# Kernel tuning notes

Measured on AMD Instinct MI355X. Metric: run time of the kernel, lower is better.

Reference implementation:

```python
import jax, jax.numpy as jnp
import numpy as np


def setup_inputs() -> dict:
    key = jax.random.key(0)
    ks = jax.random.split(key, 6)
    B, T, U = 4, 160, 80
    De, Dd = 640, 640
    inner, vocab = 640, 1024
    return {
        "enc_state": jax.random.normal(ks[0], (B, T, De), jnp.float32),
        "dec_state": jax.random.normal(ks[1], (B, U, Dd), jnp.float32),
        "W1": jax.random.normal(ks[2], (De + Dd, inner), jnp.float32) * (1.0 / np.sqrt(De + Dd)),
        "b1": jax.random.normal(ks[3], (inner,), jnp.float32) * 0.02,
        "W2": jax.random.normal(ks[4], (inner, vocab), jnp.float32) * (1.0 / np.sqrt(inner)),
        "b2": jax.random.normal(ks[5], (vocab,), jnp.float32) * 0.02,
    }


def reference(enc_state, dec_state, W1, b1, W2, b2):
    # Faithful to: cat([enc tiled over U, dec tiled over T], -1) @ W1 + b1,
    # algebraically split so the [B,T,U,2D] concat is never materialized:
    # cat(e, d) @ W1 == e @ W1[:De] + d @ W1[De:]
    De = enc_state.shape[-1]
    W1_enc, W1_dec = W1[:De], W1[De:]
    enc_proj = jnp.einsum("btd,dh->bth", enc_state, W1_enc)   # [B,T,H]
    dec_proj = jnp.einsum("bud,dh->buh", dec_state, W1_dec)   # [B,U,H]
    # broadcast add over the (T,U) lattice -> [B,T,U,H]
    hidden = jnp.tanh(enc_proj[:, :, None, :] + dec_proj[:, None, :, :] + b1)
    logits = jnp.einsum("btuh,hv->btuv", hidden, W2) + b2     # [B,T,U,V]
    return logits
```

## Files before the change

kernel.cpp:

```cpp
#include <hip/hip_runtime.h>
#include <hip/hip_bf16.h>
#include <cstdint>

#define B_    4
#define T_    160
#define U_    80
#define D_    640
#define V_    1024
#define BT_   640
#define BU_   320
#define M_    51200

typedef __bf16 bf16x8 __attribute__((ext_vector_type(8)));
typedef float floatx4 __attribute__((ext_vector_type(4)));

__device__ __forceinline__ void g2l16(const void* g, void* l) {
    __builtin_amdgcn_global_load_lds((const __attribute__((address_space(1))) void*)g,
                                     (__attribute__((address_space(3))) void*)l,
                                     16, 0, 0);
}

__device__ __forceinline__ float fast_tanh(float x) {
    float e = __builtin_amdgcn_exp2f(x * 2.8853900817779268f);
    return 1.0f - 2.0f * __builtin_amdgcn_rcpf(e + 1.0f);
}

__global__ __launch_bounds__(256) void proj_kernel(
    const float* __restrict__ enc, const float* __restrict__ dec,
    const float* __restrict__ W1,
    float* __restrict__ encp, float* __restrict__ decp) {
    __shared__ float As[64][36];
    __shared__ float Ws[32][68];

    const int rt = blockIdx.y;
    const int ct = blockIdx.x;
    const float* Asrc; const float* Wsrc; float* Cdst;
    if (rt < 10) { Asrc = enc + (size_t)rt * 64 * D_;        Wsrc = W1;           Cdst = encp + (size_t)rt * 64 * D_; }
    else         { Asrc = dec + (size_t)(rt - 10) * 64 * D_; Wsrc = W1 + D_ * D_; Cdst = decp + (size_t)(rt - 10) * 64 * D_; }

    const int tid = threadIdx.x;
    const int ar = tid >> 2,  ac = (tid & 3) * 8;
    const int wr2 = tid >> 3, wc2 = (tid & 7) * 8;
    const int tr = tid >> 4,  tc = tid & 15;

    float acc[4][4] = {};
    for (int k0 = 0; k0 < D_; k0 += 32) {
        __syncthreads();
        *(floatx4*)&As[ar][ac]       = *(const floatx4*)&Asrc[(size_t)ar * D_ + k0 + ac];
        *(floatx4*)&As[ar][ac + 4]   = *(const floatx4*)&Asrc[(size_t)ar * D_ + k0 + ac + 4];
        *(floatx4*)&Ws[wr2][wc2]     = *(const floatx4*)&Wsrc[(size_t)(k0 + wr2) * D_ + ct * 64 + wc2];
        *(floatx4*)&Ws[wr2][wc2 + 4] = *(const floatx4*)&Wsrc[(size_t)(k0 + wr2) * D_ + ct * 64 + wc2 + 4];
        __syncthreads();
#pragma unroll
        for (int kk = 0; kk < 32; kk++) {
            floatx4 w = *(const floatx4*)&Ws[kk][tc * 4];
            float a0 = As[tr * 4 + 0][kk], a1 = As[tr * 4 + 1][kk];
            float a2 = As[tr * 4 + 2][kk], a3 = As[tr * 4 + 3][kk];
#pragma unroll
            for (int j = 0; j < 4; j++) {
                acc[0][j] += a0 * w[j]; acc[1][j] += a1 * w[j];
                acc[2][j] += a2 * w[j]; acc[3][j] += a3 * w[j];
            }
        }
    }
#pragma unroll
    for (int i = 0; i < 4; i++) {
        floatx4 v = { acc[i][0], acc[i][1], acc[i][2], acc[i][3] };
        *(floatx4*)&Cdst[(size_t)(tr * 4 + i) * D_ + ct * 64 + tc * 4] = v;
    }
}

__global__ __launch_bounds__(256) void w2t_kernel(
    const float* __restrict__ W2, __bf16* __restrict__ W2t) {
    __shared__ __bf16 tile[32][33];
    const int vt = blockIdx.x;
    const int kt = blockIdx.y;
    const int tx = threadIdx.x & 31, ty = threadIdx.x >> 5;
#pragma unroll
    for (int i = 0; i < 4; i++)
        tile[ty + i * 8][tx] = (__bf16)W2[(size_t)(kt * 32 + ty + i * 8) * V_ + vt * 32 + tx];
    __syncthreads();
#pragma unroll
    for (int i = 0; i < 4; i++)
        W2t[(size_t)(vt * 32 + ty + i * 8) * D_ + kt * 32 + tx] = tile[tx][ty + i * 8];
}

__global__ __launch_bounds__(256) void hidden_kernel(
    const float* __restrict__ encp, const float* __restrict__ decp,
    const float* __restrict__ b1, __bf16* __restrict__ H) {
    const unsigned g = blockIdx.x * 256u + threadIdx.x;
    const unsigned row = g / 80u;
    const unsigned hg  = g % 80u;
    const unsigned u   = row % 80u;
    const unsigned bt  = row / 80u;
    const unsigned b   = bt / 160u;

    const float* ep = encp + (size_t)bt * D_ + hg * 8;
    const float* dp = decp + (size_t)(b * 80u + u) * D_ + hg * 8;
    const float* bp = b1 + hg * 8;

    floatx4 e0 = *(const floatx4*)ep,       e1 = *(const floatx4*)(ep + 4);
    floatx4 d0 = *(const floatx4*)dp,       d1 = *(const floatx4*)(dp + 4);
    floatx4 c0 = *(const floatx4*)bp,       c1 = *(const floatx4*)(bp + 4);

    bf16x8 hv;
#pragma unroll
    for (int i = 0; i < 4; i++) hv[i]     = (__bf16)fast_tanh(e0[i] + d0[i] + c0[i]);
#pragma unroll
    for (int i = 0; i < 4; i++) hv[i + 4] = (__bf16)fast_tanh(e1[i] + d1[i] + c1[i]);

    *(bf16x8*)(H + (size_t)g * 8) = hv;
}

#define VM4  asm volatile("s_waitcnt vmcnt(4)" ::: "memory")
#define VM0  asm volatile("s_waitcnt vmcnt(0)" ::: "memory")
#define BAR  __builtin_amdgcn_s_barrier()
#define SCB  __builtin_amdgcn_sched_barrier(0)

#define STG_A(BUF, S, TL) do { \
    g2l16(Hb + (unsigned)((S)*163840 + (TL)*128) + agl,         ldsp + (BUF)*32768 + (S)*16384 + stl); \
    g2l16(Hb + (unsigned)((S)*163840 + (TL)*128 + 10240) + agl, ldsp + (BUF)*32768 + (S)*16384 + stl + 1024); \
  } while (0)
#define STG_B(BUF, S, TL) do { \
    g2l16(Wb + (unsigned)((S)*163840 + (TL)*128) + agl,         ldsp + 65536 + (BUF)*32768 + (S)*16384 + stl); \
    g2l16(Wb + (unsigned)((S)*163840 + (TL)*128 + 10240) + agl, ldsp + 65536 + (BUF)*32768 + (S)*16384 + stl + 1024); \
  } while (0)

#define RD_A(ABUF, QM) do { \
    _Pragma("unroll") for (int ii = 0; ii < 4; ++ii) { \
      af0[ii] = *(const bf16x8*)(ldsp + (ABUF)*32768 + (QM)*16384 + ii*2048 + aRowB + sx0); \
      af1[ii] = *(const bf16x8*)(ldsp + (ABUF)*32768 + (QM)*16384 + ii*2048 + aRowB + sx1); \
    } } while (0)
#define RD_B(BG0, BG1, BBUF, QN) do { \
    _Pragma("unroll") for (int jj = 0; jj < 2; ++jj) { \
      BG0[jj] = *(const bf16x8*)(ldsp + 65536 + (BBUF)*32768 + (QN)*16384 + jj*2048 + bRowB + sx0); \
      BG1[jj] = *(const bf16x8*)(ldsp + 65536 + (BBUF)*32768 + (QN)*16384 + jj*2048 + bRowB + sx1); \
    } } while (0)
#define MM(QM, QN, BG0, BG1) do { \
    __builtin_amdgcn_s_setprio(1); \
    _Pragma("unroll") for (int ii = 0; ii < 4; ++ii) \
      _Pragma("unroll") for (int jj = 0; jj < 2; ++jj) { \
        acc[(QM)*4+ii][(QN)*2+jj] = __builtin_amdgcn_mfma_f32_16x16x32_bf16(af0[ii], BG0[jj], acc[(QM)*4+ii][(QN)*2+jj], 0, 0, 0); \
        acc[(QM)*4+ii][(QN)*2+jj] = __builtin_amdgcn_mfma_f32_16x16x32_bf16(af1[ii], BG1[jj], acc[(QM)*4+ii][(QN)*2+jj], 0, 0, 0); \
      } \
    __builtin_amdgcn_s_setprio(0); \
  } while (0)

__global__ __launch_bounds__(512, 2) void gemm_kernel(
    const __bf16* __restrict__ H, const __bf16* __restrict__ W2t,
    const float* __restrict__ b2, float* __restrict__ C) {
    __shared__ __align__(128) char lds[131072];

    const int bid = blockIdx.x;
    const int swz = (bid & 7) * 100 + (bid >> 3);
    const int mt = swz >> 2, nt = swz & 3;
    const int m0 = mt * 256, n0 = nt * 256;

    const int tid = threadIdx.x;
    const int w = tid >> 6, l = tid & 63;
    const int wr = w >> 2, wc = w & 3;
    const int lrow = l & 15, lk = l >> 4, l7 = l & 7, lhi = l >> 3;

    const unsigned swzb = (unsigned)(((l & 7) ^ lhi) * 16);
    const unsigned agl  = (unsigned)((w * 16 + lhi) * 1280) + swzb;
    const unsigned stl  = (unsigned)(w * 2048 + l * 16);

    const char* Hb = (const char*)H   + (size_t)m0 * 1280;
    const char* Wb = (const char*)W2t + (size_t)n0 * 1280;
    char* ldsp = (char*)lds;

    const unsigned aRowB = (unsigned)((wr * 64 + lrow) * 128);
    const unsigned bRowB = (unsigned)(wc * 4096 + lrow * 128);
    const unsigned sx0 = (unsigned)(((0 + lk) ^ l7) * 16);
    const unsigned sx1 = (unsigned)(((4 + lk) ^ l7) * 16);

    floatx4 acc[8][4] = {};

    STG_A(0, 0, 0); STG_A(0, 1, 0); STG_B(0, 0, 0); STG_B(0, 1, 0);
    STG_A(1, 0, 1); STG_B(1, 0, 1);
    VM4; BAR; SCB;

#pragma unroll 1
    for (int it = 0; it < 5; ++it) {
        const int t1 = 2 * it + 1, t2 = 2 * it + 2, t3 = 2 * it + 3;
        const bool pf = (it < 4);
        bf16x8 af0[4], af1[4], bgA0[2], bgA1[2], bgB0[2], bgB1[2];

        RD_A(0, 0); RD_B(bgA0, bgA1, 0, 0);
        STG_A(1, 1, t1); STG_B(1, 1, t1);
        BAR; SCB; MM(0, 0, bgA0, bgA1); BAR; SCB;
        RD_B(bgB0, bgB1, 0, 1);
        BAR; SCB; MM(0, 1, bgB0, bgB1); BAR; SCB;
        RD_A(0, 1);
        if (pf) STG_A(0, 0, t2);
        BAR; SCB; MM(1, 0, bgA0, bgA1); BAR; SCB;
        if (pf) STG_B(0, 0, t2);
        if (it == 4) { VM0; } else { VM4; }
        BAR; SCB; MM(1, 1, bgB0, bgB1); BAR; SCB;

        RD_A(1, 0); RD_B(bgA0, bgA1, 1, 0);
        if (pf) { STG_A(0, 1, t2); STG_B(0, 1, t2); }
        BAR; SCB; MM(0, 0, bgA0, bgA1); BAR; SCB;
        RD_B(bgB0, bgB1, 1, 1);
        BAR; SCB; MM(0, 1, bgB0, bgB1); BAR; SCB;
        RD_A(1, 1);
        if (pf) STG_A(1, 0, t3);
        BAR; SCB; MM(1, 0, bgA0, bgA1); BAR; SCB;
        if (pf) STG_B(1, 0, t3);
        VM4;
        BAR; SCB; MM(1, 1, bgB0, bgB1); BAR; SCB;
    }

#pragma unroll
    for (int j = 0; j < 4; ++j) {
        const int col = n0 + (j >> 1) * 128 + wc * 32 + (j & 1) * 16 + lrow;
        const float bj = b2[col];
#pragma unroll
        for (int i = 0; i < 8; ++i) {
            const int row = m0 + (i >> 2) * 128 + wr * 64 + (i & 3) * 16 + lk * 4;
            float* Cp = C + (size_t)row * V_ + col;
#pragma unroll
            for (int rg = 0; rg < 4; ++rg)
                Cp[(size_t)rg * V_] = acc[i][j][rg] + bj;
        }
    }
}

extern "C" void kernel_launch(void* const* d_in, const int* in_sizes, int n_in,
                              void* d_out, int out_size, void* d_ws, size_t ws_size,
                              hipStream_t stream) {
    const float* enc = (const float*)d_in[0];
    const float* dec = (const float*)d_in[1];
    const float* W1  = (const float*)d_in[2];
    const float* b1  = (const float*)d_in[3];
    const float* W2  = (const float*)d_in[4];
    const float* b2  = (const float*)d_in[5];
    float* out = (float*)d_out;

    char* ws = (char*)d_ws;
    float*  encp = (float*)ws;
    float*  decp = (float*)(ws + 1638400);
    __bf16* W2t  = (__bf16*)(ws + 1638400 + 819200);
    __bf16* Hbuf = (__bf16*)(ws + 1638400 + 819200 + 1310720);

    proj_kernel<<<dim3(10, 15), 256, 0, stream>>>(enc, dec, W1, encp, decp);
    w2t_kernel<<<dim3(32, 20), 256, 0, stream>>>(W2, W2t);
    hidden_kernel<<<16000, 256, 0, stream>>>(encp, decp, b1, Hbuf);
    gemm_kernel<<<800, 512, 0, stream>>>(Hbuf, W2t, b2, out);
}
```

Baseline: 355.9 us.

## Fuse tanh hidden computation into GEMM and reuse output tail as scratch

The separate hidden kernel is removed. Each GEMM block now computes tanh(enc_proj + dec_proj + b1) for its 128-row A tile directly into LDS, pipelined with W2t staging, so the bf16 H matrix is never written to or read back from global memory. The M tile shrinks to 128 rows to make room in LDS, which lowers data reuse per block. Scratch buffers (projections, W2t, counters) now live in the tail of the output buffer. Blocks writing rows that overlap that scratch spin-wait on atomic counters until every block has finished reading, which assumes forward progress of all 1600 blocks.

New measurement: 482.4 us. 35.6% more time.

```diff
diff --git a/kernel.cpp b/kernel.cpp
--- a/kernel.cpp
+++ b/kernel.cpp
@@ -2,14 +2,18 @@
 #include <hip/hip_bf16.h>
 #include <cstdint>
 
-#define B_    4
-#define T_    160
-#define U_    80
 #define D_    640
 #define V_    1024
-#define BT_   640
-#define BU_   320
 #define M_    51200
+
+#define SCR_BASE  205946880u
+#define CNT1_OFF  205946864u
+#define CNT2_OFF  205946868u
+#define ENCP_OFF  (SCR_BASE)
+#define DECP_OFF  (SCR_BASE + 1638400u)
+#define W2T_OFF   (SCR_BASE + 2457600u)
+#define NBLK      1600
+#define GATED_MT  392
 
 typedef __bf16 bf16x8 __attribute__((ext_vector_type(8)));
 typedef float floatx4 __attribute__((ext_vector_type(4)));
@@ -71,7 +75,12 @@
 }
 
 __global__ __launch_bounds__(256) void w2t_kernel(
-    const float* __restrict__ W2, __bf16* __restrict__ W2t) {
+    const float* __restrict__ W2, __bf16* __restrict__ W2t,
+    unsigned* __restrict__ cnt1, unsigned* __restrict__ cnt2) {
+    if (blockIdx.x == 0 && blockIdx.y == 0 && threadIdx.x == 0) {
+        __hip_atomic_store(cnt1, 0u, __ATOMIC_RELEASE, __HIP_MEMORY_SCOPE_AGENT);
+        __hip_atomic_store(cnt2, 0u, __ATOMIC_RELEASE, __HIP_MEMORY_SCOPE_AGENT);
+    }
     __shared__ __bf16 tile[32][33];
     const int vt = blockIdx.x;
     const int kt = blockIdx.y;
@@ -85,139 +94,135 @@
         W2t[(size_t)(vt * 32 + ty + i * 8) * D_ + kt * 32 + tx] = tile[tx][ty + i * 8];
 }
 
-__global__ __launch_bounds__(256) void hidden_kernel(
+#define STG_B(BUF, S, TL) do { \
+    g2l16(Wb + (unsigned)((S)*163840 + (TL)*128) + agl,         ldsp + 32768 + (BUF)*32768 + (S)*16384 + stl); \
+    g2l16(Wb + (unsigned)((S)*163840 + (TL)*128 + 10240) + agl, ldsp + 32768 + (BUF)*32768 + (S)*16384 + stl + 1024); \
+  } while (0)
+
+__global__ __launch_bounds__(512, 2) void joint_kernel(
     const float* __restrict__ encp, const float* __restrict__ decp,
-    const float* __restrict__ b1, __bf16* __restrict__ H) {
-    const unsigned g = blockIdx.x * 256u + threadIdx.x;
-    const unsigned row = g / 80u;
-    const unsigned hg  = g % 80u;
-    const unsigned u   = row % 80u;
-    const unsigned bt  = row / 80u;
-    const unsigned b   = bt / 160u;
-
-    const float* ep = encp + (size_t)bt * D_ + hg * 8;
-    const float* dp = decp + (size_t)(b * 80u + u) * D_ + hg * 8;
-    const float* bp = b1 + hg * 8;
-
-    floatx4 e0 = *(const floatx4*)ep,       e1 = *(const floatx4*)(ep + 4);
-    floatx4 d0 = *(const floatx4*)dp,       d1 = *(const floatx4*)(dp + 4);
-    floatx4 c0 = *(const floatx4*)bp,       c1 = *(const floatx4*)(bp + 4);
-
-    bf16x8 hv;
-#pragma unroll
-    for (int i = 0; i < 4; i++) hv[i]     = (__bf16)fast_tanh(e0[i] + d0[i] + c0[i]);
-#pragma unroll
-    for (int i = 0; i < 4; i++) hv[i + 4] = (__bf16)fast_tanh(e1[i] + d1[i] + c1[i]);
-
-    *(bf16x8*)(H + (size_t)g * 8) = hv;
-}
-
-#define VM4  asm volatile("s_waitcnt vmcnt(4)" ::: "memory")
-#define VM0  asm volatile("s_waitcnt vmcnt(0)" ::: "memory")
-#define BAR  __builtin_amdgcn_s_barrier()
-#define SCB  __builtin_amdgcn_sched_barrier(0)
-
-#define STG_A(BUF, S, TL) do { \
-    g2l16(Hb + (unsigned)((S)*163840 + (TL)*128) + agl,         ldsp + (BUF)*32768 + (S)*16384 + stl); \
-    g2l16(Hb + (unsigned)((S)*163840 + (TL)*128 + 10240) + agl, ldsp + (BUF)*32768 + (S)*16384 + stl + 1024); \
-  } while (0)
-#define STG_B(BUF, S, TL) do { \
-    g2l16(Wb + (unsigned)((S)*163840 + (TL)*128) + agl,         ldsp + 65536 + (BUF)*32768 + (S)*16384 + stl); \
-    g2l16(Wb + (unsigned)((S)*163840 + (TL)*128 + 10240) + agl, ldsp + 65536 + (BUF)*32768 + (S)*16384 + stl + 1024); \
-  } while (0)
-
-#define RD_A(ABUF, QM) do { \
-    _Pragma("unroll") for (int ii = 0; ii < 4; ++ii) { \
-      af0[ii] = *(const bf16x8*)(ldsp + (ABUF)*32768 + (QM)*16384 + ii*2048 + aRowB + sx0); \
-      af1[ii] = *(const bf16x8*)(ldsp + (ABUF)*32768 + (QM)*16384 + ii*2048 + aRowB + sx1); \
-    } } while (0)
-#define RD_B(BG0, BG1, BBUF, QN) do { \
-    _Pragma("unroll") for (int jj = 0; jj < 2; ++jj) { \
-      BG0[jj] = *(const bf16x8*)(ldsp + 65536 + (BBUF)*32768 + (QN)*16384 + jj*2048 + bRowB + sx0); \
-      BG1[jj] = *(const bf16x8*)(ldsp + 65536 + (BBUF)*32768 + (QN)*16384 + jj*2048 + bRowB + sx1); \
-    } } while (0)
-#define MM(QM, QN, BG0, BG1) do { \
-    __builtin_amdgcn_s_setprio(1); \
-    _Pragma("unroll") for (int ii = 0; ii < 4; ++ii) \
-      _Pragma("unroll") for (int jj = 0; jj < 2; ++jj) { \
-        acc[(QM)*4+ii][(QN)*2+jj] = __builtin_amdgcn_mfma_f32_16x16x32_bf16(af0[ii], BG0[jj], acc[(QM)*4+ii][(QN)*2+jj], 0, 0, 0); \
-        acc[(QM)*4+ii][(QN)*2+jj] = __builtin_amdgcn_mfma_f32_16x16x32_bf16(af1[ii], BG1[jj], acc[(QM)*4+ii][(QN)*2+jj], 0, 0, 0); \
-      } \
-    __builtin_amdgcn_s_setprio(0); \
-  } while (0)
-
-__global__ __launch_bounds__(512, 2) void gemm_kernel(
-    const __bf16* __restrict__ H, const __bf16* __restrict__ W2t,
-    const float* __restrict__ b2, float* __restrict__ C) {
-    __shared__ __align__(128) char lds[131072];
+    const float* __restrict__ b1, const __bf16* __restrict__ W2t,
+    const float* __restrict__ b2, float* __restrict__ C,
+    unsigned* __restrict__ cnt1, unsigned* __restrict__ cnt2) {
+    __shared__ __align__(128) char lds[98304];
 
     const int bid = blockIdx.x;
-    const int swz = (bid & 7) * 100 + (bid >> 3);
+    const int swz = (bid & 7) * 200 + (bid >> 3);
     const int mt = swz >> 2, nt = swz & 3;
-    const int m0 = mt * 256, n0 = nt * 256;
+    const int m0 = mt * 128, n0 = nt * 256;
 
     const int tid = threadIdx.x;
     const int w = tid >> 6, l = tid & 63;
     const int wr = w >> 2, wc = w & 3;
-    const int lrow = l & 15, lk = l >> 4, l7 = l & 7, lhi = l >> 3;
-
-    const unsigned swzb = (unsigned)(((l & 7) ^ lhi) * 16);
-    const unsigned agl  = (unsigned)((w * 16 + lhi) * 1280) + swzb;
-    const unsigned stl  = (unsigned)(w * 2048 + l * 16);
-
-    const char* Hb = (const char*)H   + (size_t)m0 * 1280;
+    const int lr = l & 15, lk = l >> 4, l7 = l & 7, lhi = l >> 3;
+
+    const unsigned agl = (unsigned)((w * 16 + lhi) * 1280) + (unsigned)(((l & 7) ^ lhi) * 16);
+    const unsigned stl = (unsigned)(w * 2048 + l * 16);
     const char* Wb = (const char*)W2t + (size_t)n0 * 1280;
     char* ldsp = (char*)lds;
 
-    const unsigned aRowB = (unsigned)((wr * 64 + lrow) * 128);
-    const unsigned bRowB = (unsigned)(wc * 4096 + lrow * 128);
-    const unsigned sx0 = (unsigned)(((0 + lk) ^ l7) * 16);
-    const unsigned sx1 = (unsigned)(((4 + lk) ^ l7) * 16);
-
-    floatx4 acc[8][4] = {};
-
-    STG_A(0, 0, 0); STG_A(0, 1, 0); STG_B(0, 0, 0); STG_B(0, 1, 0);
-    STG_A(1, 0, 1); STG_B(1, 0, 1);
-    VM4; BAR; SCB;
+    const int pr = tid >> 2;
+    const int pk = (tid & 3) * 16;
+    const int R  = m0 + pr;
+    const int bt = R / 80;
+    const int uu = R - bt * 80;
+    const int drw = (bt / 160) * 80 + uu;
+    const float* ep = encp + (size_t)bt * D_ + pk;
+    const float* dp = decp + (size_t)drw * D_ + pk;
+    const float* bp = b1 + pk;
+    const int ps = (tid & 3) * 2;
+    const unsigned pw0 = (unsigned)(pr * 128 + ((ps ^ (pr & 7)) * 16));
+    const unsigned pw1 = (unsigned)(pr * 128 + (((ps + 1) ^ (pr & 7)) * 16));
+
+    floatx4 acc[4][4] = {};
+
+    STG_B(0, 0, 0); STG_B(0, 1, 0);
+    {
+        floatx4 e0 = *(const floatx4*)(ep + 0),  e1 = *(const floatx4*)(ep + 4);
+        floatx4 e2 = *(const floatx4*)(ep + 8),  e3 = *(const floatx4*)(ep + 12);
+        floatx4 d0 = *(const floatx4*)(dp + 0),  d1 = *(const floatx4*)(dp + 4);
+        floatx4 d2 = *(const floatx4*)(dp + 8),  d3 = *(const floatx4*)(dp + 12);
+        floatx4 c0 = *(const floatx4*)(bp + 0),  c1 = *(const floatx4*)(bp + 4);
+        floatx4 c2 = *(const floatx4*)(bp + 8),  c3 = *(const floatx4*)(bp + 12);
+        bf16x8 h0, h1;
+#pragma unroll
+        for (int i = 0; i < 4; i++) { h0[i] = (__bf16)fast_tanh(e0[i] + d0[i] + c0[i]);
+                                      h0[i+4] = (__bf16)fast_tanh(e1[i] + d1[i] + c1[i]);
+                                      h1[i] = (__bf16)fast_tanh(e2[i] + d2[i] + c2[i]);
+                                      h1[i+4] = (__bf16)fast_tanh(e3[i] + d3[i] + c3[i]); }
+        *(bf16x8*)(ldsp + pw0) = h0;
+        *(bf16x8*)(ldsp + pw1) = h1;
+    }
+    __syncthreads();
 
 #pragma unroll 1
-    for (int it = 0; it < 5; ++it) {
-        const int t1 = 2 * it + 1, t2 = 2 * it + 2, t3 = 2 * it + 3;
-        const bool pf = (it < 4);
-        bf16x8 af0[4], af1[4], bgA0[2], bgA1[2], bgB0[2], bgB1[2];
-
-        RD_A(0, 0); RD_B(bgA0, bgA1, 0, 0);
-        STG_A(1, 1, t1); STG_B(1, 1, t1);
-        BAR; SCB; MM(0, 0, bgA0, bgA1); BAR; SCB;
-        RD_B(bgB0, bgB1, 0, 1);
-        BAR; SCB; MM(0, 1, bgB0, bgB1); BAR; SCB;
-        RD_A(0, 1);
-        if (pf) STG_A(0, 0, t2);
-        BAR; SCB; MM(1, 0, bgA0, bgA1); BAR; SCB;
-        if (pf) STG_B(0, 0, t2);
-        if (it == 4) { VM0; } else { VM4; }
-        BAR; SCB; MM(1, 1, bgB0, bgB1); BAR; SCB;
-
-        RD_A(1, 0); RD_B(bgA0, bgA1, 1, 0);
-        if (pf) { STG_A(0, 1, t2); STG_B(0, 1, t2); }
-        BAR; SCB; MM(0, 0, bgA0, bgA1); BAR; SCB;
-        RD_B(bgB0, bgB1, 1, 1);
-        BAR; SCB; MM(0, 1, bgB0, bgB1); BAR; SCB;
-        RD_A(1, 1);
-        if (pf) STG_A(1, 0, t3);
-        BAR; SCB; MM(1, 0, bgA0, bgA1); BAR; SCB;
-        if (pf) STG_B(1, 0, t3);
-        VM4;
-        BAR; SCB; MM(1, 1, bgB0, bgB1); BAR; SCB;
-    }
+    for (int t = 0; t < 10; ++t) {
+        const int buf = t & 1, nb = buf ^ 1;
+        floatx4 e0, e1, e2, e3, d0, d1, d2, d3, c0, c1, c2, c3;
+        if (t < 9) {
+            STG_B(nb, 0, t + 1); STG_B(nb, 1, t + 1);
+            const float* ept = ep + (t + 1) * 64;
+            const float* dpt = dp + (t + 1) * 64;
+            const float* bpt = bp + (t + 1) * 64;
+            e0 = *(const floatx4*)(ept + 0);  e1 = *(const floatx4*)(ept + 4);
+            e2 = *(const floatx4*)(ept + 8);  e3 = *(const floatx4*)(ept + 12);
+            d0 = *(const floatx4*)(dpt + 0);  d1 = *(const floatx4*)(dpt + 4);
+            d2 = *(const floatx4*)(dpt + 8);  d3 = *(const floatx4*)(dpt + 12);
+            c0 = *(const floatx4*)(bpt + 0);  c1 = *(const floatx4*)(bpt + 4);
+            c2 = *(const floatx4*)(bpt + 8);  c3 = *(const floatx4*)(bpt + 12);
+        }
+#pragma unroll
+        for (int s = 0; s < 2; ++s) {
+            bf16x8 af[4], bfr[4];
+            const unsigned sx = (unsigned)(((s * 4 + lk) ^ l7) * 16);
+#pragma unroll
+            for (int i = 0; i < 4; ++i)
+                af[i] = *(const bf16x8*)(ldsp + buf * 16384 + (wr * 64 + i * 16 + lr) * 128 + sx);
+#pragma unroll
+            for (int j = 0; j < 4; ++j)
+                bfr[j] = *(const bf16x8*)(ldsp + 32768 + buf * 32768 + (wc * 64 + j * 16 + lr) * 128 + sx);
+#pragma unroll
+            for (int i = 0; i < 4; ++i)
+#pragma unroll
+                for (int j = 0; j < 4; ++j)
+                    acc[i][j] = __builtin_amdgcn_mfma_f32_16x16x32_bf16(af[i], bfr[j], acc[i][j], 0, 0, 0);
+        }
+        if (t < 9) {
+            bf16x8 h0, h1;
+#pragma unroll
+            for (int i = 0; i < 4; i++) { h0[i] = (__bf16)fast_tanh(e0[i] + d0[i] + c0[i]);
+                                          h0[i+4] = (__bf16)fast_tanh(e1[i] + d1[i] + c1[i]);
+                                          h1[i] = (__bf16)fast_tanh(e2[i] + d2[i] + c2[i]);
+                                          h1[i+4] = (__bf16)fast_tanh(e3[i] + d3[i] + c3[i]); }
+            *(bf16x8*)(ldsp + nb * 16384 + pw0) = h0;
+            *(bf16x8*)(ldsp + nb * 16384 + pw1) = h1;
+        }
+        __syncthreads();
+    }
+
+    asm volatile("s_waitcnt vmcnt(0) lgkmcnt(0)" ::: "memory");
+    __syncthreads();
+    if (tid == 0) {
+        __hip_atomic_fetch_add(cnt1, 1u, __ATOMIC_ACQ_REL, __HIP_MEMORY_SCOPE_AGENT);
+        if (mt >= GATED_MT) {
+            while (__hip_atomic_load(cnt1, __ATOMIC_ACQUIRE, __HIP_MEMORY_SCOPE_AGENT) < NBLK)
+                __builtin_amdgcn_s_sleep(8);
+            __hip_atomic_fetch_add(cnt2, 1u, __ATOMIC_ACQ_REL, __HIP_MEMORY_SCOPE_AGENT);
+            if (mt == GATED_MT && nt == 3) {
+                while (__hip_atomic_load(cnt2, __ATOMIC_ACQUIRE, __HIP_MEMORY_SCOPE_AGENT) < 32u)
+                    __builtin_amdgcn_s_sleep(8);
+            }
+        }
+    }
+    __syncthreads();
 
 #pragma unroll
     for (int j = 0; j < 4; ++j) {
-        const int col = n0 + (j >> 1) * 128 + wc * 32 + (j & 1) * 16 + lrow;
+        const int col = n0 + wc * 64 + j * 16 + lr;
         const float bj = b2[col];
 #pragma unroll
-        for (int i = 0; i < 8; ++i) {
-            const int row = m0 + (i >> 2) * 128 + wr * 64 + (i & 3) * 16 + lk * 4;
+        for (int i = 0; i < 4; ++i) {
+            const int row = m0 + wr * 64 + i * 16 + lk * 4;
             float* Cp = C + (size_t)row * V_ + col;
 #pragma unroll
             for (int rg = 0; rg < 4; ++rg)
@@ -237,14 +242,14 @@
     const float* b2  = (const float*)d_in[5];
     float* out = (float*)d_out;
 
-    char* ws = (char*)d_ws;
-    float*  encp = (float*)ws;
-    float*  decp = (float*)(ws + 1638400);
-    __bf16* W2t  = (__bf16*)(ws + 1638400 + 819200);
-    __bf16* Hbuf = (__bf16*)(ws + 1638400 + 819200 + 1310720);
+    char* ob = (char*)d_out;
+    float*    encp = (float*)(ob + ENCP_OFF);
+    float*    decp = (float*)(ob + DECP_OFF);
+    __bf16*   W2t  = (__bf16*)(ob + W2T_OFF);
+    unsigned* cnt1 = (unsigned*)(ob + CNT1_OFF);
+    unsigned* cnt2 = (unsigned*)(ob + CNT2_OFF);
 
     proj_kernel<<<dim3(10, 15), 256, 0, stream>>>(enc, dec, W1, encp, decp);
-    w2t_kernel<<<dim3(32, 20), 256, 0, stream>>>(W2, W2t);
-    hidden_kernel<<<16000, 256, 0, stream>>>(encp, decp, b1, Hbuf);
-    gemm_kernel<<<800, 512, 0, stream>>>(Hbuf, W2t, b2, out);
-}
+    w2t_kernel<<<dim3(32, 20), 256, 0, stream>>>(W2, W2t, cnt1, cnt2);
+    joint_kernel<<<1600, 512, 0, stream>>>(encp, decp, b1, W2t, b2, out, cnt1, cnt2);
+}
```

## Fold b1 into encoder projection and reorder GEMM quadrant schedule for finer staging

Applied to the files above, without the earlier changes.

The b1 bias add moves into the encoder projection epilogue, so the hidden kernel no longer loads b1. The GEMM main loop now walks the four 128x128 quadrants in a serpentine order, reloading A or B fragments alternately, which removes one set of B fragment registers. Global-to-LDS staging is spread across more phases, and the wait count rises from 4 to 6 so more loads stay in flight. The risk is a race or stale-buffer read if the new wait placement does not cover every LDS region before it is read.

Result: no change. 352.4 us (-1.0%).

```diff
diff --git a/kernel.cpp b/kernel.cpp
--- a/kernel.cpp
+++ b/kernel.cpp
@@ -2,13 +2,8 @@
 #include <hip/hip_bf16.h>
 #include <cstdint>
 
-#define B_    4
-#define T_    160
-#define U_    80
 #define D_    640
 #define V_    1024
-#define BT_   640
-#define BU_   320
 #define M_    51200
 
 typedef __bf16 bf16x8 __attribute__((ext_vector_type(8)));
@@ -27,16 +22,17 @@
 
 __global__ __launch_bounds__(256) void proj_kernel(
     const float* __restrict__ enc, const float* __restrict__ dec,
-    const float* __restrict__ W1,
+    const float* __restrict__ W1, const float* __restrict__ b1,
     float* __restrict__ encp, float* __restrict__ decp) {
     __shared__ float As[64][36];
     __shared__ float Ws[32][68];
 
     const int rt = blockIdx.y;
     const int ct = blockIdx.x;
+    const bool is_enc = (rt < 10);
     const float* Asrc; const float* Wsrc; float* Cdst;
-    if (rt < 10) { Asrc = enc + (size_t)rt * 64 * D_;        Wsrc = W1;           Cdst = encp + (size_t)rt * 64 * D_; }
-    else         { Asrc = dec + (size_t)(rt - 10) * 64 * D_; Wsrc = W1 + D_ * D_; Cdst = decp + (size_t)(rt - 10) * 64 * D_; }
+    if (is_enc) { Asrc = enc + (size_t)rt * 64 * D_;        Wsrc = W1;           Cdst = encp + (size_t)rt * 64 * D_; }
+    else        { Asrc = dec + (size_t)(rt - 10) * 64 * D_; Wsrc = W1 + D_ * D_; Cdst = decp + (size_t)(rt - 10) * 64 * D_; }
 
     const int tid = threadIdx.x;
     const int ar = tid >> 2,  ac = (tid & 3) * 8;
@@ -63,9 +59,12 @@
             }
         }
     }
+    floatx4 bv = {0.f, 0.f, 0.f, 0.f};
+    if (is_enc) bv = *(const floatx4*)&b1[ct * 64 + tc * 4];
 #pragma unroll
     for (int i = 0; i < 4; i++) {
-        floatx4 v = { acc[i][0], acc[i][1], acc[i][2], acc[i][3] };
+        floatx4 v = { acc[i][0] + bv[0], acc[i][1] + bv[1],
+                      acc[i][2] + bv[2], acc[i][3] + bv[3] };
         *(floatx4*)&Cdst[(size_t)(tr * 4 + i) * D_ + ct * 64 + tc * 4] = v;
     }
 }
@@ -87,7 +86,7 @@
 
 __global__ __launch_bounds__(256) void hidden_kernel(
     const float* __restrict__ encp, const float* __restrict__ decp,
-    const float* __restrict__ b1, __bf16* __restrict__ H) {
+    __bf16* __restrict__ H) {
     const unsigned g = blockIdx.x * 256u + threadIdx.x;
     const unsigned row = g / 80u;
     const unsigned hg  = g % 80u;
@@ -97,22 +96,20 @@
 
     const float* ep = encp + (size_t)bt * D_ + hg * 8;
     const float* dp = decp + (size_t)(b * 80u + u) * D_ + hg * 8;
-    const float* bp = b1 + hg * 8;
-
-    floatx4 e0 = *(const floatx4*)ep,       e1 = *(const floatx4*)(ep + 4);
-    floatx4 d0 = *(const floatx4*)dp,       d1 = *(const floatx4*)(dp + 4);
-    floatx4 c0 = *(const floatx4*)bp,       c1 = *(const floatx4*)(bp + 4);
+
+    floatx4 e0 = *(const floatx4*)ep, e1 = *(const floatx4*)(ep + 4);
+    floatx4 d0 = *(const floatx4*)dp, d1 = *(const floatx4*)(dp + 4);
 
     bf16x8 hv;
 #pragma unroll
-    for (int i = 0; i < 4; i++) hv[i]     = (__bf16)fast_tanh(e0[i] + d0[i] + c0[i]);
-#pragma unroll
-    for (int i = 0; i < 4; i++) hv[i + 4] = (__bf16)fast_tanh(e1[i] + d1[i] + c1[i]);
+    for (int i = 0; i < 4; i++) hv[i]     = (__bf16)fast_tanh(e0[i] + d0[i]);
+#pragma unroll
+    for (int i = 0; i < 4; i++) hv[i + 4] = (__bf16)fast_tanh(e1[i] + d1[i]);
 
     *(bf16x8*)(H + (size_t)g * 8) = hv;
 }
 
-#define VM4  asm volatile("s_waitcnt vmcnt(4)" ::: "memory")
+#define VM6  asm volatile("s_waitcnt vmcnt(6)" ::: "memory")
 #define VM0  asm volatile("s_waitcnt vmcnt(0)" ::: "memory")
 #define BAR  __builtin_amdgcn_s_barrier()
 #define SCB  __builtin_amdgcn_sched_barrier(0)
@@ -131,17 +128,17 @@
       af0[ii] = *(const bf16x8*)(ldsp + (ABUF)*32768 + (QM)*16384 + ii*2048 + aRowB + sx0); \
       af1[ii] = *(const bf16x8*)(ldsp + (ABUF)*32768 + (QM)*16384 + ii*2048 + aRowB + sx1); \
     } } while (0)
-#define RD_B(BG0, BG1, BBUF, QN) do { \
+#define RD_B(BBUF, QN) do { \
     _Pragma("unroll") for (int jj = 0; jj < 2; ++jj) { \
-      BG0[jj] = *(const bf16x8*)(ldsp + 65536 + (BBUF)*32768 + (QN)*16384 + jj*2048 + bRowB + sx0); \
-      BG1[jj] = *(const bf16x8*)(ldsp + 65536 + (BBUF)*32768 + (QN)*16384 + jj*2048 + bRowB + sx1); \
+      bg0[jj] = *(const bf16x8*)(ldsp + 65536 + (BBUF)*32768 + (QN)*16384 + jj*2048 + bRowB + sx0); \
+      bg1[jj] = *(const bf16x8*)(ldsp + 65536 + (BBUF)*32768 + (QN)*16384 + jj*2048 + bRowB + sx1); \
     } } while (0)
-#define MM(QM, QN, BG0, BG1) do { \
+#define MM(QM, QN) do { \
     __builtin_amdgcn_s_setprio(1); \
     _Pragma("unroll") for (int ii = 0; ii < 4; ++ii) \
       _Pragma("unroll") for (int jj = 0; jj < 2; ++jj) { \
-        acc[(QM)*4+ii][(QN)*2+jj] = __builtin_amdgcn_mfma_f32_16x16x32_bf16(af0[ii], BG0[jj], acc[(QM)*4+ii][(QN)*2+jj], 0, 0, 0); \
-        acc[(QM)*4+ii][(QN)*2+jj] = __builtin_amdgcn_mfma_f32_16x16x32_bf16(af1[ii], BG1[jj], acc[(QM)*4+ii][(QN)*2+jj], 0, 0, 0); \
+        acc[(QM)*4+ii][(QN)*2+jj] = __builtin_amdgcn_mfma_f32_16x16x32_bf16(af0[ii], bg0[jj], acc[(QM)*4+ii][(QN)*2+jj], 0, 0, 0); \
+        acc[(QM)*4+ii][(QN)*2+jj] = __builtin_amdgcn_mfma_f32_16x16x32_bf16(af1[ii], bg1[jj], acc[(QM)*4+ii][(QN)*2+jj], 0, 0, 0); \
       } \
     __builtin_amdgcn_s_setprio(0); \
   } while (0)
@@ -176,39 +173,49 @@
 
     floatx4 acc[8][4] = {};
 
-    STG_A(0, 0, 0); STG_A(0, 1, 0); STG_B(0, 0, 0); STG_B(0, 1, 0);
-    STG_A(1, 0, 1); STG_B(1, 0, 1);
-    VM4; BAR; SCB;
+    STG_A(0, 0, 0); STG_B(0, 0, 0); STG_A(0, 1, 0); STG_B(0, 1, 0);
+    STG_B(1, 0, 1); STG_A(1, 1, 1); STG_B(1, 1, 1);
+    VM6; BAR; SCB;
 
 #pragma unroll 1
     for (int it = 0; it < 5; ++it) {
         const int t1 = 2 * it + 1, t2 = 2 * it + 2, t3 = 2 * it + 3;
-        const bool pf = (it < 4);
-        bf16x8 af0[4], af1[4], bgA0[2], bgA1[2], bgB0[2], bgB1[2];
-
-        RD_A(0, 0); RD_B(bgA0, bgA1, 0, 0);
-        STG_A(1, 1, t1); STG_B(1, 1, t1);
-        BAR; SCB; MM(0, 0, bgA0, bgA1); BAR; SCB;
-        RD_B(bgB0, bgB1, 0, 1);
-        BAR; SCB; MM(0, 1, bgB0, bgB1); BAR; SCB;
+        const bool g = (it < 4);
+        bf16x8 af0[4], af1[4], bg0[2], bg1[2];
+
+        RD_A(0, 0); RD_B(0, 0);
+        STG_A(1, 0, t1);
+        BAR; SCB; MM(0, 0); BAR; SCB;
+
         RD_A(0, 1);
-        if (pf) STG_A(0, 0, t2);
-        BAR; SCB; MM(1, 0, bgA0, bgA1); BAR; SCB;
-        if (pf) STG_B(0, 0, t2);
-        if (it == 4) { VM0; } else { VM4; }
-        BAR; SCB; MM(1, 1, bgB0, bgB1); BAR; SCB;
-
-        RD_A(1, 0); RD_B(bgA0, bgA1, 1, 0);
-        if (pf) { STG_A(0, 1, t2); STG_B(0, 1, t2); }
-        BAR; SCB; MM(0, 0, bgA0, bgA1); BAR; SCB;
-        RD_B(bgB0, bgB1, 1, 1);
-        BAR; SCB; MM(0, 1, bgB0, bgB1); BAR; SCB;
+        if (g) STG_B(0, 0, t2);
+        BAR; SCB; MM(1, 0); BAR; SCB;
+
+        RD_B(0, 1);
+        if (g) STG_A(0, 1, t2);
+        BAR; SCB; MM(1, 1); BAR; SCB;
+
+        RD_A(0, 0);
+        if (g) STG_B(0, 1, t2);
+        if (it == 4) { VM0; } else { VM6; }
+        BAR; SCB; MM(0, 1); BAR; SCB;
+
+        RD_A(1, 0); RD_B(1, 0);
+        if (g) STG_A(0, 0, t2);
+        BAR; SCB; MM(0, 0); BAR; SCB;
+
         RD_A(1, 1);
-        if (pf) STG_A(1, 0, t3);
-        BAR; SCB; MM(1, 0, bgA0, bgA1); BAR; SCB;
-        if (pf) STG_B(1, 0, t3);
-        VM4;
-        BAR; SCB; MM(1, 1, bgB0, bgB1); BAR; SCB;
+        if (g) STG_B(1, 0, t3);
+        BAR; SCB; MM(1, 0); BAR; SCB;
+
+        RD_B(1, 1);
+        if (g) STG_A(1, 1, t3);
+        BAR; SCB; MM(1, 1); BAR; SCB;
+
+        RD_A(1, 0);
+        if (g) STG_B(1, 1, t3);
+        if (g) { VM6; }
+        BAR; SCB; MM(0, 1); BAR; SCB;
     }
 
 #pragma unroll
@@ -243,8 +250,8 @@
     __bf16* W2t  = (__bf16*)(ws + 1638400 + 819200);
     __bf16* Hbuf = (__bf16*)(ws + 1638400 + 819200 + 1310720);
 
-    proj_kernel<<<dim3(10, 15), 256, 0, stream>>>(enc, dec, W1, encp, decp);
+    proj_kernel<<<dim3(10, 15), 256, 0, stream>>>(enc, dec, W1, b1, encp, decp);
     w2t_kernel<<<dim3(32, 20), 256, 0, stream>>>(W2, W2t);
-    hidden_kernel<<<16000, 256, 0, stream>>>(encp, decp, b1, Hbuf);
+    hidden_kernel<<<16000, 256, 0, stream>>>(encp, decp, Hbuf);
     gemm_kernel<<<800, 512, 0, stream>>>(Hbuf, W2t, b2, out);
 }
```
